# Kernel tuning notes

Hardware: AMD Instinct MI355X
Metric: run time of the kernel (lower is better)

## Reference

```python
import jax, jax.numpy as jnp
import numpy as np

S, B, E, H = 2048, 64, 256, 256

def setup_inputs() -> dict:
    key = jax.random.key(0)
    k1, k2, k3, k4, k5 = jax.random.split(key, 5)
    scale = 1.0 / np.sqrt(H)
    return {
        "sentence": jax.random.normal(k1, (S, B, E), dtype=jnp.float32),
        "h0": jax.random.uniform(k2, (B, H), dtype=jnp.float32),
        "W_ih": jax.random.normal(k3, (E, H), dtype=jnp.float32) * scale,
        "W_hh": jax.random.normal(k4, (H, H), dtype=jnp.float32) * scale,
        "b": jax.random.normal(k5, (H,), dtype=jnp.float32) * scale,
    }

def reference(sentence, h0, W_ih, W_hh, b):
    # Precompute input projections for all steps in one big GEMM: [S,B,H]
    x_proj = jnp.einsum("sbe,eh->sbh", sentence, W_ih) + b

    def step(h, xp):
        h_new = jnp.tanh(xp + h @ W_hh)  # [B,H]
        return h_new, None

    h_final, _ = jax.lax.scan(step, h0, x_proj)
    return h_final  # [B,H]
```

## Files before the change

### kernel.cpp

```cpp
#include <hip/hip_runtime.h>
#include <math.h>

#define S_TOT 2048
#define B_    64
#define E_    256
#define H_    256

typedef __fp16 half2v __attribute__((ext_vector_type(2)));

__global__ __launch_bounds__(512, 2) void fused_step(
    const float* __restrict__ A,
    const float* __restrict__ Wih,
    const float* __restrict__ bias,
    float*       __restrict__ xp_next,
    const float* __restrict__ xp_cur,
    const float* __restrict__ Whh,
    float*       __restrict__ h,
    int steps, int scan_blocks)
{
    __shared__ float smem[32 * 68 + 32 * 64];
    const int tid = threadIdx.x;

    if ((int)blockIdx.x < scan_blocks) {
        float* hbuf = smem;
        const int b  = blockIdx.x;
        const int ks = tid & 7;
        const int jg = tid >> 3;
        const int j0 = jg << 2;
        const int jf = j0 + ((ks & 1) << 1) + ((ks >> 1) & 1);

        half2v w[16][4];
        #pragma unroll
        for (int i = 0; i < 16; i++) {
            const float* r0 = &Whh[(size_t)(ks * 32 + 2 * i) * H_ + j0];
            const float* r1 = r0 + H_;
            #pragma unroll
            for (int jj = 0; jj < 4; jj++) {
                half2v v = __builtin_amdgcn_cvt_pkrtz(r0[jj], r1[jj]);
                int vi = __builtin_bit_cast(int, v);
                asm volatile("" : "+v"(vi));
                w[i][jj] = __builtin_bit_cast(half2v, vi);
            }
        }

        if (tid < 128) {
            half2v hp = __builtin_amdgcn_cvt_pkrtz(h[b * H_ + 2 * tid],
                                                   h[b * H_ + 2 * tid + 1]);
            const int j = 2 * tid;
            ((half2v*)hbuf)[(j >> 5) * 20 + ((j & 31) >> 1)] = hp;
        }
        float xpn = xp_cur[(size_t)b * H_ + jf];
        __syncthreads();

        int p = 0;
        for (int s = 0; s < steps; s++) {
            const float xpc = xpn;
            if (s + 1 < steps)
                xpn = xp_cur[((size_t)(s + 1) * B_ + b) * H_ + jf];

            half2v hk[16];
            {
                const float4* hs = (const float4*)&hbuf[p * 160 + ks * 20];
                float4 t0 = hs[0], t1 = hs[1], t2 = hs[2], t3 = hs[3];
                *(float4*)&hk[0]  = t0;
                *(float4*)&hk[4]  = t1;
                *(float4*)&hk[8]  = t2;
                *(float4*)&hk[12] = t3;
            }

            float acc[4] = {0.f, 0.f, 0.f, 0.f};
            #pragma unroll
            for (int i = 0; i < 16; i++) {
                #pragma unroll
                for (int jj = 0; jj < 4; jj++)
                    acc[jj] = __builtin_amdgcn_fdot2(hk[i], w[i][jj],
                                                     acc[jj], false);
            }

            const bool b0 = (ks & 1), b1 = (ks & 2), b2 = (ks & 4);
            float r0, r1, q, v;
            {
                float s0 = b0 ? acc[0] : acc[2];
                float s1 = b0 ? acc[1] : acc[3];
                r0 = (b0 ? acc[2] : acc[0]) + __shfl_xor(s0, 1);
                r1 = (b0 ? acc[3] : acc[1]) + __shfl_xor(s1, 1);
            }
            {
                float s0 = b1 ? r0 : r1;
                q = (b1 ? r1 : r0) + __shfl_xor(s0, 2);
            }
            v = q + __shfl_xor(q, 4);

            v += xpc;
            const float e2 = __expf(2.f * v);
            const float hn = 1.f - 2.f / (e2 + 1.f);
            if (!b2) {
                ((__fp16*)hbuf)[(p ^ 1) * 320 + (jf >> 5) * 40 + (jf & 31)]
                    = (__fp16)hn;
                if (s == steps - 1) h[b * H_ + jf] = hn;
            }
            __syncthreads();
            p ^= 1;
        }
    } else if (A != nullptr) {
        float (*As)[68] = (float(*)[68])smem;
        float (*Bs)[64] = (float(*)[64])(smem + 32 * 68);

        const int gid = blockIdx.x - scan_blocks;
        const int bm = (gid >> 2) * 64;
        const int bn = (gid & 3) * 64;
        const int tx = tid & 15;
        const int ty = tid >> 4;

        float acc[2][4] = {};

        const int ar = tid >> 3;
        const int ak = (tid & 7) << 2;
        const int br = tid >> 4;
        const int bc = (tid & 15) << 2;

        for (int k0 = 0; k0 < E_; k0 += 32) {
            float4 a0  = *(const float4*)&A[(size_t)(bm + ar) * E_ + k0 + ak];
            float4 bv0 = *(const float4*)&Wih[(size_t)(k0 + br) * H_ + bn + bc];

            As[ak+0][ar] = a0.x; As[ak+1][ar] = a0.y;
            As[ak+2][ar] = a0.z; As[ak+3][ar] = a0.w;
            *(float4*)&Bs[br][bc] = bv0;
            __syncthreads();

            #pragma unroll
            for (int kk = 0; kk < 32; kk++) {
                const float2 av = *(const float2*)&As[kk][ty << 1];
                const float4 bv = *(const float4*)&Bs[kk][tx << 2];
                acc[0][0] += av.x*bv.x; acc[0][1] += av.x*bv.y;
                acc[0][2] += av.x*bv.z; acc[0][3] += av.x*bv.w;
                acc[1][0] += av.y*bv.x; acc[1][1] += av.y*bv.y;
                acc[1][2] += av.y*bv.z; acc[1][3] += av.y*bv.w;
            }
            __syncthreads();
        }

        const float4 bb = *(const float4*)&bias[bn + (tx << 2)];
        #pragma unroll
        for (int i = 0; i < 2; i++) {
            float4 o;
            o.x = acc[i][0] + bb.x;
            o.y = acc[i][1] + bb.y;
            o.z = acc[i][2] + bb.z;
            o.w = acc[i][3] + bb.w;
            *(float4*)&xp_next[(size_t)(bm + (ty << 1) + i) * H_ + bn + (tx << 2)] = o;
        }
    }
}

extern "C" void kernel_launch(void* const* d_in, const int* in_sizes, int n_in,
                              void* d_out, int out_size, void* d_ws, size_t ws_size,
                              hipStream_t stream)
{
    const float* sentence = (const float*)d_in[0];
    const float* h0       = (const float*)d_in[1];
    const float* W_ih     = (const float*)d_in[2];
    const float* W_hh     = (const float*)d_in[3];
    const float* bias     = (const float*)d_in[4];
    float* h  = (float*)d_out;
    float* ws = (float*)d_ws;

    int chunk = 256;
    while ((size_t)2 * chunk * B_ * H_ * sizeof(float) > ws_size && chunk > 32)
        chunk >>= 1;
    const int nchunk = S_TOT / chunk;
    float* buf[2] = { ws, ws + (size_t)chunk * B_ * H_ };

    hipMemcpyAsync(h, h0, B_ * H_ * sizeof(float), hipMemcpyDeviceToDevice, stream);

    fused_step<<<chunk * 4, 512, 0, stream>>>(sentence, W_ih, bias, buf[0],
                                              nullptr, W_hh, h, 0, 0);
    for (int c = 0; c < nchunk; c++) {
        const bool last = (c == nchunk - 1);
        const int gemmb = last ? 0 : chunk * 4;
        const float* Anext = last ? nullptr
                                  : sentence + (size_t)(c + 1) * chunk * B_ * E_;
        fused_step<<<64 + gemmb, 512, 0, stream>>>(Anext, W_ih, bias,
                                                   buf[(c + 1) & 1],
                                                   buf[c & 1], W_hh, h,
                                                   chunk, 64);
    }
}
```

Measured before the change: 1.502 ms.

## Repartition RNN scan to 4-way K split with DPP reductions

```diff
diff --git a/kernel.cpp b/kernel.cpp
--- a/kernel.cpp
+++ b/kernel.cpp
@@ -7,6 +7,17 @@
 #define H_    256
 
 typedef __fp16 half2v __attribute__((ext_vector_type(2)));
+
+__device__ __forceinline__ float dpp_xor1(float x) {
+    int i = __builtin_bit_cast(int, x);
+    i = __builtin_amdgcn_mov_dpp(i, 0xB1, 0xF, 0xF, true);
+    return __builtin_bit_cast(float, i);
+}
+__device__ __forceinline__ float dpp_xor2(float x) {
+    int i = __builtin_bit_cast(int, x);
+    i = __builtin_amdgcn_mov_dpp(i, 0x4E, 0xF, 0xF, true);
+    return __builtin_bit_cast(float, i);
+}
 
 __global__ __launch_bounds__(512, 2) void fused_step(
     const float* __restrict__ A,
@@ -24,18 +35,18 @@
     if ((int)blockIdx.x < scan_blocks) {
         float* hbuf = smem;
         const int b  = blockIdx.x;
-        const int ks = tid & 7;
-        const int jg = tid >> 3;
-        const int j0 = jg << 2;
-        const int jf = j0 + ((ks & 1) << 1) + ((ks >> 1) & 1);
+        const int ks = tid & 3;
+        const int jg = tid >> 2;
+        const int j0 = jg << 1;
+        const int jf = j0 + (ks & 1);
 
-        half2v w[16][4];
+        half2v w[32][2];
         #pragma unroll
-        for (int i = 0; i < 16; i++) {
-            const float* r0 = &Whh[(size_t)(ks * 32 + 2 * i) * H_ + j0];
+        for (int i = 0; i < 32; i++) {
+            const float* r0 = &Whh[(size_t)(ks * 64 + 2 * i) * H_ + j0];
             const float* r1 = r0 + H_;
             #pragma unroll
-            for (int jj = 0; jj < 4; jj++) {
+            for (int jj = 0; jj < 2; jj++) {
                 half2v v = __builtin_amdgcn_cvt_pkrtz(r0[jj], r1[jj]);
                 int vi = __builtin_bit_cast(int, v);
                 asm volatile("" : "+v"(vi));
@@ -46,58 +57,56 @@
         if (tid < 128) {
             half2v hp = __builtin_amdgcn_cvt_pkrtz(h[b * H_ + 2 * tid],
                                                    h[b * H_ + 2 * tid + 1]);
-            const int j = 2 * tid;
-            ((half2v*)hbuf)[(j >> 5) * 20 + ((j & 31) >> 1)] = hp;
+            ((half2v*)hbuf)[(tid >> 5) * 36 + (tid & 31)] = hp;
         }
         float xpn = xp_cur[(size_t)b * H_ + jf];
         __syncthreads();
 
         int p = 0;
+        const int rd_base = ks * 36;
+        const int wr_idx  = (jg >> 5) * 36 + (jg & 31);
         for (int s = 0; s < steps; s++) {
             const float xpc = xpn;
             if (s + 1 < steps)
                 xpn = xp_cur[((size_t)(s + 1) * B_ + b) * H_ + jf];
 
-            half2v hk[16];
+            half2v hk[32];
             {
-                const float4* hs = (const float4*)&hbuf[p * 160 + ks * 20];
-                float4 t0 = hs[0], t1 = hs[1], t2 = hs[2], t3 = hs[3];
-                *(float4*)&hk[0]  = t0;
-                *(float4*)&hk[4]  = t1;
-                *(float4*)&hk[8]  = t2;
-                *(float4*)&hk[12] = t3;
+                const float4* hs = (const float4*)&hbuf[p * 144 + rd_base];
+                #pragma unroll
+                for (int t = 0; t < 8; t++)
+                    *(float4*)&hk[t * 4] = hs[t];
             }
 
-            float acc[4] = {0.f, 0.f, 0.f, 0.f};
+            float p00 = 0.f, p01 = 0.f, p10 = 0.f, p11 = 0.f;
             #pragma unroll
             for (int i = 0; i < 16; i++) {
-                #pragma unroll
-                for (int jj = 0; jj < 4; jj++)
-                    acc[jj] = __builtin_amdgcn_fdot2(hk[i], w[i][jj],
-                                                     acc[jj], false);
+                p00 = __builtin_amdgcn_fdot2(hk[i], w[i][0], p00, false);
+                p01 = __builtin_amdgcn_fdot2(hk[i], w[i][1], p01, false);
             }
+            #pragma unroll
+            for (int i = 16; i < 32; i++) {
+                p10 = __builtin_amdgcn_fdot2(hk[i], w[i][0], p10, false);
+                p11 = __builtin_amdgcn_fdot2(hk[i], w[i][1], p11, false);
+            }
+            const float acc0 = p00 + p10;
+            const float acc1 = p01 + p11;
 
-            const bool b0 = (ks & 1), b1 = (ks & 2), b2 = (ks & 4);
-            float r0, r1, q, v;
-            {
-                float s0 = b0 ? acc[0] : acc[2];
-                float s1 = b0 ? acc[1] : acc[3];
-                r0 = (b0 ? acc[2] : acc[0]) + __shfl_xor(s0, 1);
-                r1 = (b0 ? acc[3] : acc[1]) + __shfl_xor(s1, 1);
-            }
-            {
-                float s0 = b1 ? r0 : r1;
-                q = (b1 ? r1 : r0) + __shfl_xor(s0, 2);
-            }
-            v = q + __shfl_xor(q, 4);
+            const bool b0 = (ks & 1);
+            const float r = (b0 ? acc1 : acc0) + dpp_xor1(b0 ? acc0 : acc1);
+            const float v = r + dpp_xor2(r) + xpc;
 
-            v += xpc;
             const float e2 = __expf(2.f * v);
             const float hn = 1.f - 2.f / (e2 + 1.f);
-            if (!b2) {
-                ((__fp16*)hbuf)[(p ^ 1) * 320 + (jf >> 5) * 40 + (jf & 31)]
-                    = (__fp16)hn;
-                if (s == steps - 1) h[b * H_ + jf] = hn;
+
+            const float other = dpp_xor1(hn);
+            if (ks == 0) {
+                ((half2v*)hbuf)[(p ^ 1) * 144 + wr_idx] =
+                    __builtin_amdgcn_cvt_pkrtz(hn, other);
+                if (s == steps - 1) {
+                    float2 o; o.x = hn; o.y = other;
+                    *(float2*)&h[b * H_ + j0] = o;
+                }
             }
             __syncthreads();
             p ^= 1;
```

New measurement: 1.324 ms. -11.8%, faster.
